# Kernel tuning notes

Hardware: AMD Instinct MI355X
Metric: run time of the kernel (lower is better)

## Reference

```python
import jax, jax.numpy as jnp
import numpy as np
from jax import lax


def setup_inputs() -> dict:
    key = jax.random.key(0)
    k1, k2, k3, k4 = jax.random.split(key, 4)
    H = 2048
    L = 3
    hidden_states = jax.random.normal(k1, (2, 4096, H), dtype=jnp.float32)
    Win = jax.random.normal(k2, (3 * H, H), dtype=jnp.float32) * (H ** -0.5)
    conv_w = jax.random.normal(k3, (H, 1, L), dtype=jnp.float32) * (L ** -0.5)
    Wout = jax.random.normal(k4, (H, H), dtype=jnp.float32) * (H ** -0.5)
    return {"hidden_states": hidden_states, "Win": Win, "conv_w": conv_w, "Wout": Wout}


def reference(hidden_states, Win, conv_w, Wout):
    H = hidden_states.shape[-1]
    L = conv_w.shape[-1]
    BCx = jnp.einsum('bsh,oh->bso', hidden_states, Win)  # (b, s, 3H)
    B, C, x = jnp.split(BCx, 3, axis=-1)
    Bx = jnp.transpose(B * x, (0, 2, 1))  # (b, H, s)
    # depthwise causal conv: left-pad L-1 so output length == s (torch pads both
    # sides then slices [..., :seqlen]; left-only padding is equivalent)
    conv_out = lax.conv_general_dilated(
        Bx, conv_w, window_strides=(1,), padding=[(L - 1, 0)],
        feature_group_count=H, dimension_numbers=('NCH', 'OIH', 'NCH'))
    y = C * jnp.transpose(conv_out, (0, 2, 1))  # (b, s, H)
    return jnp.einsum('bsh,oh->bso', y, Wout)
```

## Files before the change

### kernel.cpp

```cpp
#include <hip/hip_runtime.h>
#include <hip/hip_bf16.h>

typedef unsigned short u16;
typedef __attribute__((ext_vector_type(8))) short bf16x8;
typedef __attribute__((ext_vector_type(4))) float f32x4;

static __device__ __forceinline__ u16 f2bf(float f) {
    unsigned u = __float_as_uint(f);
    unsigned r = (u + 0x7fffu + ((u >> 16) & 1u)) >> 16;
    return (u16)r;
}
static __device__ __forceinline__ float bf2f(u16 u) {
    return __uint_as_float(((unsigned)u) << 16);
}

static __device__ __forceinline__ void async_copy16(const void* gptr, void* lptr) {
    __builtin_amdgcn_global_load_lds(
        (const __attribute__((address_space(1))) void*)gptr,
        (__attribute__((address_space(3))) void*)lptr, 16, 0, 0);
}

__global__ __launch_bounds__(256)
void cvt_all(const float* __restrict__ a, const float* __restrict__ b,
             const float* __restrict__ c,
             u16* __restrict__ oa, u16* __restrict__ ob, u16* __restrict__ oc) {
    int blk = blockIdx.x;
    const float* src; u16* dst; long base;
    if (blk < 16384)      { src = a; dst = oa; base = blk; }
    else if (blk < 28672) { src = b; dst = ob; base = blk - 16384; }
    else                  { src = c; dst = oc; base = blk - 28672; }
    long i = (base * 256 + threadIdx.x) * 4;
    float4 f = *(const float4*)(src + i);
    u16 o[4] = { f2bf(f.x), f2bf(f.y), f2bf(f.z), f2bf(f.w) };
    *(uint2*)(dst + i) = *(const uint2*)o;
}

template<bool BF16_OUT>
__global__ __launch_bounds__(512, 2)
void gemm_bt8(const u16* __restrict__ A, const u16* __restrict__ B,
              void* __restrict__ Cout, int M, int N, int K) {
    __shared__ __align__(16) u16 lds[65536];

    const int t    = threadIdx.x;
    const int lane = t & 63;
    const int wm   = (t >> 6) >> 2;
    const int wn   = (t >> 6) & 3;
    const int l15  = lane & 15;
    const int hi   = lane >> 4;
    const int l7   = lane & 7;

    const int id   = blockIdx.y * gridDim.x + blockIdx.x;
    const int cpx  = gridDim.x >> 3;
    const int bx   = (id & 7) * cpx + ((id >> 3) % cpx);
    const int by   = (id >> 3) / cpx;
    const long rowA = (long)by * 256;
    const long rowB = (long)bx * 256;

    const int pl0 = t >> 3;
    const int slotcol = ((t & 7) ^ (pl0 & 7)) * 8;
    const u16* Asrc[2][2]; const u16* Bsrc[2][2];
#pragma unroll
    for (int h = 0; h < 2; h++) {
        int gA0 = h * 64 + pl0;
        int gA1 = 128 + h * 64 + pl0;
        Asrc[h][0] = A + (rowA + gA0) * (long)K + slotcol;
        Asrc[h][1] = A + (rowA + gA1) * (long)K + slotcol;
        int nB0 = (pl0 >> 5) * 64 + h * 32 + (pl0 & 31);
        Bsrc[h][0] = B + (rowB + nB0) * (long)K + slotcol;
        Bsrc[h][1] = B + (rowB + nB0 + 128) * (long)K + slotcol;
    }
    const int t8 = t * 8;

    auto STAGE_A = [&](int bufo, int h, int kk) {
        u16* d = lds + bufo + h * 8192 + t8;
        async_copy16(Asrc[h][0] + kk, d);
        async_copy16(Asrc[h][1] + kk, d + 4096);
    };
    auto STAGE_B = [&](int bufo, int h, int kk) {
        u16* d = lds + bufo + 16384 + h * 8192 + t8;
        async_copy16(Bsrc[h][0] + kk, d);
        async_copy16(Bsrc[h][1] + kk, d + 4096);
    };

    const int aBase = wm * 4096 + l15 * 64;
    const int bBase = 16384 + wn * 2048 + l15 * 64;
    const int sOff0 = (hi ^ l7) * 8;
    const int sOff1 = ((4 + hi) ^ l7) * 8;

    bf16x8 af[4][2], ba[2][2], bb[2][2];
    f32x4 acc[8][4] = {};

    auto LOAD_A2 = [&](int bufo, int Mq, int mb) {
        const u16* p = lds + bufo + Mq * 8192 + aBase + mb * 1024;
        af[mb][0]     = *(const bf16x8*)(p + sOff0);
        af[mb][1]     = *(const bf16x8*)(p + sOff1);
        af[mb + 1][0] = *(const bf16x8*)(p + 1024 + sOff0);
        af[mb + 1][1] = *(const bf16x8*)(p + 1024 + sOff1);
    };
    auto LOAD_B = [&](bf16x8 (&bg)[2][2], int bufo, int Nq) {
        const u16* p = lds + bufo + Nq * 8192 + bBase;
        bg[0][0] = *(const bf16x8*)(p + sOff0);
        bg[0][1] = *(const bf16x8*)(p + sOff1);
        bg[1][0] = *(const bf16x8*)(p + 1024 + sOff0);
        bg[1][1] = *(const bf16x8*)(p + 1024 + sOff1);
    };
    auto MFMA_H = [&](int Mq, int Nq, int mb, bf16x8 (&bg)[2][2]) {
        __builtin_amdgcn_s_setprio(1);
#pragma unroll
        for (int ks = 0; ks < 2; ks++)
#pragma unroll
            for (int m = mb; m < mb + 2; m++)
#pragma unroll
                for (int n = 0; n < 2; n++)
                    acc[Mq * 4 + m][Nq * 2 + n] =
                        __builtin_amdgcn_mfma_f32_16x16x32_bf16(
                            af[m][ks], bg[n][ks], acc[Mq * 4 + m][Nq * 2 + n],
                            0, 0, 0);
        __builtin_amdgcn_s_setprio(0);
    };

#define BAR()   __builtin_amdgcn_s_barrier()
#define SB()    __builtin_amdgcn_sched_barrier(0)
#define LGKM(n) do { asm volatile("s_waitcnt lgkmcnt(" #n ")" ::: "memory"); \
                     __builtin_amdgcn_sched_barrier(0); } while (0)
#define VM(n)   asm volatile("s_waitcnt vmcnt(" #n ")" ::: "memory")

#define TILE(BC, BN, KK)                                                     \
                                                              \
    LOAD_B(ba, BC, 0); LOAD_A2(BC, 0, 0); SB(); LOAD_A2(BC, 0, 2);           \
    STAGE_A(BN, 0, KK); VM(2);                                               \
    LGKM(4); MFMA_H(0, 0, 0, ba); LGKM(0); MFMA_H(0, 0, 2, ba); BAR();       \
                                                              \
    LOAD_B(bb, BC, 1);                                                       \
    STAGE_B(BN, 0, KK);                                                      \
    LGKM(0); MFMA_H(0, 1, 0, bb); MFMA_H(0, 1, 2, bb); BAR();                \
                                                              \
    LOAD_A2(BC, 1, 0); SB(); LOAD_A2(BC, 1, 2);                              \
    STAGE_A(BN, 1, KK);                                                      \
    LGKM(4); MFMA_H(1, 1, 0, bb); LGKM(0); MFMA_H(1, 1, 2, bb); BAR();       \
                                                              \
    STAGE_B(BN, 1, KK); VM(4);                                               \
    MFMA_H(1, 0, 0, ba); MFMA_H(1, 0, 2, ba); BAR();

    STAGE_A(0, 0, 0);  STAGE_B(0, 0, 0);
    STAGE_A(0, 1, 0);  STAGE_B(0, 1, 0);
    asm volatile("s_waitcnt vmcnt(0)" ::: "memory");
    BAR();

    const int NT = K >> 6;
#pragma unroll 1
    for (int i = 0; i < NT; i += 2) {
        int k1 = (i + 1) << 6;
        int k2 = (i + 2 < NT) ? (i + 2) << 6 : 0;
        TILE(0, 32768, k1);
        TILE(32768, 0, k2);
    }
    asm volatile("s_waitcnt vmcnt(0) lgkmcnt(0)" ::: "memory");

#undef TILE
#undef VM
#undef LGKM
#undef SB
#undef BAR

    const long crowBase = rowA + wm * 128 + hi * 4;
    const long ccolBase = rowB + wn * 64 + l15;
#pragma unroll
    for (int mi = 0; mi < 8; mi++) {
#pragma unroll
        for (int nj = 0; nj < 4; nj++) {
            long base = (crowBase + mi * 16) * N + ccolBase + nj * 16;
#pragma unroll
            for (int r = 0; r < 4; r++) {
                float v = acc[mi][nj][r];
                long idx = base + (long)r * N;
                if (BF16_OUT) ((u16*)Cout)[idx] = f2bf(v);
                else          ((float*)Cout)[idx] = v;
            }
        }
    }
}

union U16x8 { uint4 v; u16 u[8]; };

__global__ __launch_bounds__(256)
void conv_fuse(const u16* __restrict__ BCx, const float* __restrict__ cw,
               u16* __restrict__ y) {
    const int row = blockIdx.x;
    const int h0  = threadIdx.x * 8;
    const int sl  = row & 4095;
    const u16* r0 = BCx + (long)row * 6144;

    U16x8 B0, X0, C0, B1, X1, B2, X2;
    B0.v = *(const uint4*)(r0 + h0);
    C0.v = *(const uint4*)(r0 + 2048 + h0);
    X0.v = *(const uint4*)(r0 + 4096 + h0);
    if (sl >= 1) {
        B1.v = *(const uint4*)(r0 - 6144 + h0);
        X1.v = *(const uint4*)(r0 - 6144 + 4096 + h0);
    } else { B1.v = make_uint4(0,0,0,0); X1.v = make_uint4(0,0,0,0); }
    if (sl >= 2) {
        B2.v = *(const uint4*)(r0 - 12288 + h0);
        X2.v = *(const uint4*)(r0 - 12288 + 4096 + h0);
    } else { B2.v = make_uint4(0,0,0,0); X2.v = make_uint4(0,0,0,0); }

    U16x8 o;
#pragma unroll
    for (int i = 0; i < 8; i++) {
        int h = h0 + i;
        float bx0 = bf2f(B0.u[i]) * bf2f(X0.u[i]);
        float bx1 = bf2f(B1.u[i]) * bf2f(X1.u[i]);
        float bx2 = bf2f(B2.u[i]) * bf2f(X2.u[i]);
        float v = cw[h*3+2] * bx0 + cw[h*3+1] * bx1 + cw[h*3] * bx2;
        o.u[i] = f2bf(v * bf2f(C0.u[i]));
    }
    *(uint4*)(y + (long)row * 2048 + h0) = o.v;
}

extern "C" void kernel_launch(void* const* d_in, const int* in_sizes, int n_in,
                              void* d_out, int out_size, void* d_ws, size_t ws_size,
                              hipStream_t stream) {
    const float* hs   = (const float*)d_in[0];
    const float* Win  = (const float*)d_in[1];
    const float* cw   = (const float*)d_in[2];
    const float* Wout = (const float*)d_in[3];
    float* out = (float*)d_out;

    char* ws = (char*)d_ws;
    u16* hsb   = (u16*)(ws);
    u16* Winb  = (u16*)(ws +  33554432);
    u16* Woutb = (u16*)(ws +  58720256);
    u16* bcx   = (u16*)(ws +  67108864);
    u16* yb    = (u16*)(ws + 167772160);

    cvt_all<<<32768, 256, 0, stream>>>(hs, Win, Wout, hsb, Winb, Woutb);

    gemm_bt8<true ><<<dim3(24, 32), 512, 0, stream>>>(hsb, Winb, bcx, 8192, 6144, 2048);

    conv_fuse<<<8192, 256, 0, stream>>>(bcx, cw, yb);

    gemm_bt8<false><<<dim3(8, 32), 512, 0, stream>>>(yb, Woutb, out, 8192, 2048, 2048);
}
```

Before: 432.9 us.

## Restructure GEMM tile pipeline to prefetch next-tile LDS fragments during MFMA

```diff
diff --git a/kernel.cpp b/kernel.cpp
--- a/kernel.cpp
+++ b/kernel.cpp
@@ -90,12 +90,13 @@
     bf16x8 af[4][2], ba[2][2], bb[2][2];
     f32x4 acc[8][4] = {};
 
-    auto LOAD_A2 = [&](int bufo, int Mq, int mb) {
-        const u16* p = lds + bufo + Mq * 8192 + aBase + mb * 1024;
-        af[mb][0]     = *(const bf16x8*)(p + sOff0);
-        af[mb][1]     = *(const bf16x8*)(p + sOff1);
-        af[mb + 1][0] = *(const bf16x8*)(p + 1024 + sOff0);
-        af[mb + 1][1] = *(const bf16x8*)(p + 1024 + sOff1);
+    auto LOAD_A4 = [&](int bufo, int Mq) {
+        const u16* p = lds + bufo + Mq * 8192 + aBase;
+#pragma unroll
+        for (int m = 0; m < 4; m++) {
+            af[m][0] = *(const bf16x8*)(p + m * 1024 + sOff0);
+            af[m][1] = *(const bf16x8*)(p + m * 1024 + sOff1);
+        }
     };
     auto LOAD_B = [&](bf16x8 (&bg)[2][2], int bufo, int Nq) {
         const u16* p = lds + bufo + Nq * 8192 + bBase;
@@ -104,12 +105,12 @@
         bg[1][0] = *(const bf16x8*)(p + 1024 + sOff0);
         bg[1][1] = *(const bf16x8*)(p + 1024 + sOff1);
     };
-    auto MFMA_H = [&](int Mq, int Nq, int mb, bf16x8 (&bg)[2][2]) {
+    auto MFMA_F = [&](int Mq, int Nq, bf16x8 (&bg)[2][2]) {
         __builtin_amdgcn_s_setprio(1);
 #pragma unroll
         for (int ks = 0; ks < 2; ks++)
 #pragma unroll
-            for (int m = mb; m < mb + 2; m++)
+            for (int m = 0; m < 4; m++)
 #pragma unroll
                 for (int n = 0; n < 2; n++)
                     acc[Mq * 4 + m][Nq * 2 + n] =
@@ -126,26 +127,29 @@
 #define VM(n)   asm volatile("s_waitcnt vmcnt(" #n ")" ::: "memory")
 
 #define TILE(BC, BN, KK)                                                     \
-                                                              \
-    LOAD_B(ba, BC, 0); LOAD_A2(BC, 0, 0); SB(); LOAD_A2(BC, 0, 2);           \
-    STAGE_A(BN, 0, KK); VM(2);                                               \
-    LGKM(4); MFMA_H(0, 0, 0, ba); LGKM(0); MFMA_H(0, 0, 2, ba); BAR();       \
-                                                              \
+         \
     LOAD_B(bb, BC, 1);                                                       \
-    STAGE_B(BN, 0, KK);                                                      \
-    LGKM(0); MFMA_H(0, 1, 0, bb); MFMA_H(0, 1, 2, bb); BAR();                \
-                                                              \
-    LOAD_A2(BC, 1, 0); SB(); LOAD_A2(BC, 1, 2);                              \
-    STAGE_A(BN, 1, KK);                                                      \
-    LGKM(4); MFMA_H(1, 1, 0, bb); LGKM(0); MFMA_H(1, 1, 2, bb); BAR();       \
-                                                              \
-    STAGE_B(BN, 1, KK); VM(4);                                               \
-    MFMA_H(1, 0, 0, ba); MFMA_H(1, 0, 2, ba); BAR();
+    LGKM(4); MFMA_F(0, 0, ba);                                               \
+    VM(0); BAR();                                                            \
+                 \
+    STAGE_A(BN, 0, KK); STAGE_B(BN, 0, KK);                                  \
+    LGKM(0); MFMA_F(0, 1, bb);                                               \
+    SB(); LOAD_A4(BC, 1);                                                    \
+    BAR();                                                                   \
+              \
+    STAGE_B(BN, 1, KK); STAGE_A(BN, 1, KK);                                  \
+    LGKM(0); MFMA_F(1, 1, bb);                                               \
+    VM(4); BAR();                                                            \
+         \
+    LGKM(0); MFMA_F(1, 0, ba);                                               \
+    SB(); LOAD_B(ba, BN, 0); LOAD_A4(BN, 0);                                 \
+    VM(2); BAR();
 
     STAGE_A(0, 0, 0);  STAGE_B(0, 0, 0);
     STAGE_A(0, 1, 0);  STAGE_B(0, 1, 0);
     asm volatile("s_waitcnt vmcnt(0)" ::: "memory");
     BAR();
+    LOAD_A4(0, 0);  LOAD_B(ba, 0, 0);
 
     const int NT = K >> 6;
 #pragma unroll 1
```

Result: faster. 424.1 us (-2.0%).
